# Optimization experiments

Measured on AMD Instinct MI355X. Metric: run time of the kernel, lower is better.

The kernel has to match this reference:

```python
import jax, jax.numpy as jnp
import numpy as np

EPS = 1e-12  # torch F.normalize eps

def _l2norm(x):
    n = jnp.linalg.norm(x, axis=-1, keepdims=True)
    return x / jnp.maximum(n, EPS)

def _encode(h, mask, W, b):
    # h: [B,S,H], mask: [B,S] int
    h = h * mask[..., None].astype(h.dtype)      # zero padded tokens
    pooled = h[:, 0]                             # pooling_type='cls'
    col = h[:, 1:] @ W + b                       # colbert_linear on tokens 1:
    return _l2norm(pooled), _l2norm(col)         # normalize=True


def setup_inputs() -> dict:
    key = jax.random.key(0)
    k1, k2, k3, k4, k5, k6 = jax.random.split(key, 6)
    Q, Sq, C, Sc, H, D = 64, 32, 256, 256, 768, 128
    return {
        "q_hidden": jax.random.normal(k1, (Q, Sq, H), jnp.float32),
        "c_hidden": jax.random.normal(k2, (C, Sc, H), jnp.float32),
        "W": jax.random.normal(k3, (H, D), jnp.float32) / np.sqrt(H).astype(np.float32),
        "b": jax.random.normal(k4, (D,), jnp.float32) * 0.01,
        "q_mask": jax.random.randint(k5, (Q, Sq), 0, 2, jnp.int32),
        "c_mask": jax.random.randint(k6, (C, Sc), 0, 2, jnp.int32),
    }


def reference(q_hidden, c_hidden, W, b, q_mask, c_mask):
    q_pooled, q_col = _encode(q_hidden, q_mask, W, b)   # q_col: [Q, Sq-1, D]
    c_pooled, c_col = _encode(c_hidden, c_mask, W, b)   # c_col: [C, Sc-1, D]
    # MaxSim late interaction (get_batch_colbert_sim)
    token_sim = jnp.einsum('qin,cjn->qicj', q_col, c_col)  # [Q, Sq-1, C, Sc-1]
    sim = token_sim.max(axis=-1)                           # max over doc tokens j
    denom = q_mask[:, 1:].sum(-1, keepdims=True).astype(sim.dtype)
    sim = sim.sum(axis=1) / denom                          # [Q, C]
    return sim, q_pooled, c_pooled
```

## Files before the change

### kernel.cpp

```cpp
#include <hip/hip_runtime.h>
#include <hip/hip_bf16.h>

#define QN 64
#define SQ 32
#define CN 256
#define SC 256
#define HD 768
#define DD 128

typedef __attribute__((ext_vector_type(8))) short short8;
typedef __attribute__((ext_vector_type(4))) float f32x4;

static __device__ __forceinline__ unsigned short f2bf(float x) {
  unsigned u = __float_as_uint(x);
  unsigned r = 0x7FFFu + ((u >> 16) & 1u);
  return (unsigned short)((u + r) >> 16);
}
static __device__ __forceinline__ unsigned pack2(float a, float b) {
  return (unsigned)f2bf(a) | ((unsigned)f2bf(b) << 16);
}

typedef const __attribute__((address_space(1))) unsigned int* as1_u32p;
typedef __attribute__((address_space(3))) unsigned int* as3_u32p;
static __device__ __forceinline__ void gl_lds16(const void* g, void* l) {
  __builtin_amdgcn_global_load_lds((as1_u32p)g, (as3_u32p)l, 16, 0, 0);
}

__global__ __launch_bounds__(256) void prep_kernel(
    const float* __restrict__ W,
    const float* __restrict__ qh, const int* __restrict__ qm,
    const float* __restrict__ ch, const int* __restrict__ cm,
    unsigned short* __restrict__ WtS,
    float* __restrict__ outq, float* __restrict__ outc,
    unsigned short* __restrict__ qcolP) {
  __shared__ float red[4];
  int bid = blockIdx.x, tid = threadIdx.x;

  if (bid < DD) {
    int d = bid;
    if (tid < 96) {
      int kc = tid;
      unsigned p[4];
#pragma unroll
      for (int e = 0; e < 4; ++e) {
        float a = W[(size_t)(kc * 8 + 2 * e) * DD + d];
        float b = W[(size_t)(kc * 8 + 2 * e + 1) * DD + d];
        p[e] = pack2(a, b);
      }
      int kcp = (kc & ~7) | ((kc & 7) ^ (d & 7));
      *(uint4*)&WtS[((size_t)d * 96 + kcp) * 8] = *(uint4*)p;
    }
    return;
  }

  int row = bid - DD;
  const float* src;
  float* dst;
  float m;
  if (row < QN) {
    src = qh + (size_t)row * SQ * HD;
    m = (float)qm[row * SQ];
    dst = outq + (size_t)row * HD;
  } else {
    int b = row - QN;
    src = ch + (size_t)b * SC * HD;
    m = (float)cm[b * SC];
    dst = outc + (size_t)b * HD;
  }
  float ss = 0.f;
  for (int k = tid; k < HD; k += 256) {
    float v = src[k] * m;
    ss += v * v;
  }
  int lane = tid & 63, wv = tid >> 6;
  for (int off = 32; off; off >>= 1) ss += __shfl_xor(ss, off);
  if (lane == 0) red[wv] = ss;
  __syncthreads();
  float tot = red[0] + red[1] + red[2] + red[3];
  float inv = 1.f / fmaxf(sqrtf(tot), 1e-12f);
  for (int k = tid; k < HD; k += 256) dst[k] = src[k] * m * inv;
  if (row < QN && tid < 64)
    ((unsigned*)(qcolP + ((size_t)row * 32 + 31) * DD))[tid] = 0u;
}

union ProjLDS {
  unsigned short w[2][128 * 64];
  float cep[64 * 132];
};

__global__ __launch_bounds__(256, 2) void proj_kernel(
    const float* __restrict__ q_hidden, const float* __restrict__ c_hidden,
    const int* __restrict__ q_mask, const int* __restrict__ c_mask,
    const unsigned short* __restrict__ WtS, const float* __restrict__ bias,
    unsigned short* __restrict__ qcol, unsigned short* __restrict__ ccol) {
  __shared__ ProjLDS u;
  int bx = blockIdx.x;
  int isQ = (bx >= 510) ? 1 : 0;
  int base = isQ ? (bx - 510) : bx;
  int tid = threadIdx.x, lane = tid & 63, wv = tid >> 6;
  int lm = lane & 15, lq = lane >> 4;

  const float* abase[2];
#pragma unroll
  for (int mt = 0; mt < 2; ++mt) {
    int g = base * 128 + wv * 32 + mt * 16 + lm;
    const float* hp;
    if (isQ) {
      g = (g > 1983) ? 1983 : g;
      int qq = g / 31, t = g - qq * 31;
      hp = q_hidden + ((size_t)qq * SQ + t + 1) * HD;
    } else {
      int cb = g / 255, t = g - cb * 255;
      hp = c_hidden + ((size_t)cb * SC + t + 1) * HD;
    }
    abase[mt] = hp + lq * 8;
  }

  const unsigned short* wptr[4];
#pragma unroll
  for (int i = 0; i < 4; ++i) {
    int d = i * 32 + (tid >> 3);
    wptr[i] = WtS + ((size_t)d * 96 + (tid & 7)) * 8;
  }

  f32x4 acc[2][8];
#pragma unroll
  for (int i = 0; i < 2; ++i)
#pragma unroll
    for (int j = 0; j < 8; ++j) acc[i][j] = (f32x4){0.f, 0.f, 0.f, 0.f};

  float4 Pa[8], Pb[8];

#pragma unroll
  for (int w = 0; w < 2; ++w)
#pragma unroll
    for (int mt = 0; mt < 2; ++mt) {
      Pa[w * 4 + mt * 2 + 0] = *(const float4*)(abase[mt] + w * 32);
      Pa[w * 4 + mt * 2 + 1] = *(const float4*)(abase[mt] + w * 32 + 4);
    }
#pragma unroll
  for (int i = 0; i < 4; ++i)
    gl_lds16(wptr[i], (char*)&u.w[0][0] + (size_t)(i * 256 + wv * 64) * 16);
  __syncthreads();

#define PROJ_STEP(t, PC, PN, CB, NB, PREFETCH)                                 \
  {                                                                            \
    if (PREFETCH) {                                                            \
      _Pragma("unroll")                                                        \
      for (int w = 0; w < 2; ++w)                                              \
        _Pragma("unroll")                                                      \
        for (int mt = 0; mt < 2; ++mt) {                                       \
          PN[w * 4 + mt * 2 + 0] =                                             \
              *(const float4*)(abase[mt] + (t + 1) * 64 + w * 32);             \
          PN[w * 4 + mt * 2 + 1] =                                             \
              *(const float4*)(abase[mt] + (t + 1) * 64 + w * 32 + 4);         \
        }                                                                      \
      _Pragma("unroll")                                                        \
      for (int i = 0; i < 4; ++i)                                              \
        gl_lds16(wptr[i] + (t + 1) * 64,                                       \
                 (char*)&u.w[NB][0] + (size_t)(i * 256 + wv * 64) * 16);       \
    }                                                                          \
    _Pragma("unroll")                                                          \
    for (int w = 0; w < 2; ++w) {                                              \
      short8 afr[2];                                                           \
      _Pragma("unroll")                                                        \
      for (int mt = 0; mt < 2; ++mt) {                                         \
        float4 a0 = PC[w * 4 + mt * 2], a1 = PC[w * 4 + mt * 2 + 1];           \
        unsigned pk[4];                                                        \
        pk[0] = pack2(a0.x, a0.y); pk[1] = pack2(a0.z, a0.w);                  \
        pk[2] = pack2(a1.x, a1.y); pk[3] = pack2(a1.z, a1.w);                  \
        afr[mt] = *(short8*)pk;                                                \
      }                                                                        \
      _Pragma("unroll")                                                        \
      for (int nt = 0; nt < 8; ++nt) {                                         \
        int d = nt * 16 + lm;                                                  \
        int pc = (w * 4 + lq) ^ (lm & 7);                                      \
        short8 bfr = *(const short8*)&u.w[CB][d * 64 + pc * 8];                \
        acc[0][nt] = __builtin_amdgcn_mfma_f32_16x16x32_bf16(afr[0], bfr,      \
                                                             acc[0][nt], 0, 0, 0); \
        acc[1][nt] = __builtin_amdgcn_mfma_f32_16x16x32_bf16(afr[1], bfr,      \
                                                             acc[1][nt], 0, 0, 0); \
      }                                                                        \
    }                                                                          \
    __syncthreads();                                                           \
  }

#pragma unroll
  for (int s = 0; s < 12; s += 2) {
    PROJ_STEP(s, Pa, Pb, 0, 1, 1);
    PROJ_STEP(s + 1, Pb, Pa, 1, 0, (s + 1 < 11));
  }
#undef PROJ_STEP

  int tk = tid >> 2, qt = tid & 3;
#pragma unroll
  for (int h = 0; h < 2; ++h) {
    __syncthreads();
    if ((wv >> 1) == h) {
#pragma unroll
      for (int mt = 0; mt < 2; ++mt)
#pragma unroll
        for (int nt = 0; nt < 8; ++nt)
#pragma unroll
          for (int r = 0; r < 4; ++r) {
            int row = (wv & 1) * 32 + mt * 16 + lq * 4 + r;
            u.cep[row * 132 + nt * 16 + lm] = acc[mt][nt][r];
          }
    }
    __syncthreads();

    int g = base * 128 + h * 64 + tk;
    int qq, t, valid = 1;
    float fm;
    if (isQ) {
      if (g > 1983) { valid = 0; g = 1983; }
      qq = g / 31; t = g - qq * 31;
      fm = (float)q_mask[qq * SQ + t + 1];
    } else {
      qq = g / 255; t = g - qq * 255;
      fm = (float)c_mask[qq * SC + t + 1];
    }

    float v[32];
    float ss = 0.f;
#pragma unroll
    for (int j = 0; j < 8; ++j) {
      float4 cv = *(const float4*)&u.cep[tk * 132 + qt * 32 + j * 4];
      float4 bv = *(const float4*)&bias[qt * 32 + j * 4];
      v[4 * j + 0] = cv.x * fm + bv.x; v[4 * j + 1] = cv.y * fm + bv.y;
      v[4 * j + 2] = cv.z * fm + bv.z; v[4 * j + 3] = cv.w * fm + bv.w;
#pragma unroll
      for (int e = 0; e < 4; ++e) ss += v[4 * j + e] * v[4 * j + e];
    }
    ss += __shfl_xor(ss, 1);
    ss += __shfl_xor(ss, 2);
    float inv = 1.f / fmaxf(sqrtf(ss), 1e-12f);

    uint4 pk4[4];
#pragma unroll
    for (int j = 0; j < 4; ++j) {
      unsigned p[4];
#pragma unroll
      for (int e = 0; e < 4; ++e)
        p[e] = pack2(v[8 * j + 2 * e] * inv, v[8 * j + 2 * e + 1] * inv);
      pk4[j] = *(uint4*)p;
    }

    if (isQ) {
      if (valid) {
        uint4* dst = (uint4*)(qcol + ((size_t)qq * 32 + t) * DD + qt * 32);
#pragma unroll
        for (int j = 0; j < 4; ++j) dst[j] = pk4[j];
      }
    } else {
      uint4* rowp = (uint4*)(ccol + ((size_t)qq * 256 + t) * DD);
#pragma unroll
      for (int j = 0; j < 4; ++j) {
        int kc = qt * 4 + j;
        int p = (kc & 8) | ((kc & 7) ^ (t & 7));
        rowp[p] = pk4[j];
      }
      if (t == 254) {
        uint4* rowp2 = rowp + 16;
#pragma unroll
        for (int j = 0; j < 4; ++j) {
          int kc = qt * 4 + j;
          int p = (kc & 8) | ((kc & 7) ^ 7);
          rowp2[p] = pk4[j];
        }
      }
    }
  }
}

__global__ __launch_bounds__(256, 2) void sim_kernel(
    const unsigned short* __restrict__ qcolP,
    const unsigned short* __restrict__ ccol,
    const int* __restrict__ qmask,
    float* __restrict__ sim) {
  __shared__ unsigned short cbuf[2][128 * 128];
  int tid = threadIdx.x, lane = tid & 63, wv = tid >> 6;
  int lm = lane & 15, lq = lane >> 4;
  int qb = blockIdx.y * 16 + wv * 4;
  int c0 = blockIdx.x * 2;

  short8 af[4][2][4];
#pragma unroll
  for (int q2 = 0; q2 < 4; ++q2)
#pragma unroll
    for (int it = 0; it < 2; ++it)
#pragma unroll
      for (int kf = 0; kf < 4; ++kf)
        af[q2][it][kf] = *(const short8*)(qcolP +
            (((size_t)(qb + q2) * 32 + it * 16 + lm) * DD + kf * 32 + lq * 8));

  float dinv[4];
#pragma unroll
  for (int q2 = 0; q2 < 4; ++q2) {
    float v = (lane >= 1 && lane < 32) ? (float)qmask[(qb + q2) * SQ + lane] : 0.f;
    for (int off = 1; off < 64; off <<= 1) v += __shfl_xor(v, off);
    dinv[q2] = 1.f / v;
  }

  const unsigned short* csrc = ccol + (size_t)c0 * SC * DD;

#pragma unroll
  for (int i = 0; i < 8; ++i)
    gl_lds16(csrc + (size_t)(i * 256 + tid) * 8,
             (char*)&cbuf[0][0] + (size_t)(i * 256 + wv * 64) * 16);
  __syncthreads();

  float rmax[4][2];
  for (int ht = 0; ht < 4; ++ht) {
    int b = ht & 1;
    if (!(ht & 1)) {
#pragma unroll
      for (int q2 = 0; q2 < 4; ++q2) {
        rmax[q2][0] = -__builtin_inff();
        rmax[q2][1] = -__builtin_inff();
      }
    }
    if (ht < 3) {
      const unsigned short* s2 = csrc + (size_t)(ht + 1) * 16384;
#pragma unroll
      for (int i = 0; i < 8; ++i)
        gl_lds16(s2 + (size_t)(i * 256 + tid) * 8,
                 (char*)&cbuf[b ^ 1][0] + (size_t)(i * 256 + wv * 64) * 16);
    }

    for (int jt = 0; jt < 8; ++jt) {
      short8 cf[4];
#pragma unroll
      for (int kf = 0; kf < 4; ++kf) {
        int row = jt * 16 + lm;
        int kc = kf * 4 + lq;
        int p = (kc & 8) | ((kc & 7) ^ (row & 7));
        cf[kf] = *(const short8*)&cbuf[b][(size_t)(row * 16 + p) * 8];
      }
#pragma unroll
      for (int q2 = 0; q2 < 4; ++q2)
#pragma unroll
        for (int it = 0; it < 2; ++it) {
          f32x4 acc = (f32x4){0.f, 0.f, 0.f, 0.f};
#pragma unroll
          for (int kf = 0; kf < 4; ++kf)
            acc = __builtin_amdgcn_mfma_f32_16x16x32_bf16(cf[kf], af[q2][it][kf], acc, 0, 0, 0);
          float loc = fmaxf(fmaxf(acc[0], acc[1]), fmaxf(acc[2], acc[3]));
          rmax[q2][it] = fmaxf(rmax[q2][it], loc);
        }
    }

    if (ht & 1) {
      int c = c0 + (ht >> 1);
#pragma unroll
      for (int q2 = 0; q2 < 4; ++q2) {
        float m0 = rmax[q2][0], m1 = rmax[q2][1];
        m0 = fmaxf(m0, __shfl_xor(m0, 16)); m0 = fmaxf(m0, __shfl_xor(m0, 32));
        m1 = fmaxf(m1, __shfl_xor(m1, 16)); m1 = fmaxf(m1, __shfl_xor(m1, 32));
        float s = m0 + ((lm == 15) ? 0.f : m1);
        s += __shfl_xor(s, 1); s += __shfl_xor(s, 2);
        s += __shfl_xor(s, 4); s += __shfl_xor(s, 8);
        if (lane == 0) sim[(qb + q2) * CN + c] = s * dinv[q2];
      }
    }
    __syncthreads();
  }
}

extern "C" void kernel_launch(void* const* d_in, const int* in_sizes, int n_in,
                              void* d_out, int out_size, void* d_ws, size_t ws_size,
                              hipStream_t stream) {
  const float* q_hidden = (const float*)d_in[0];
  const float* c_hidden = (const float*)d_in[1];
  const float* W = (const float*)d_in[2];
  const float* bias = (const float*)d_in[3];
  const int* q_mask = (const int*)d_in[4];
  const int* c_mask = (const int*)d_in[5];

  float* out = (float*)d_out;
  float* sim = out;
  float* q_pooled = out + QN * CN;
  float* c_pooled = q_pooled + QN * HD;

  unsigned short* WtS   = (unsigned short*)d_ws;
  unsigned short* qcolP = (unsigned short*)((char*)d_ws + (256 << 10));
  unsigned short* ccol  = (unsigned short*)((char*)d_ws + (1 << 20));

  prep_kernel<<<DD + QN + CN, 256, 0, stream>>>(W, q_hidden, q_mask, c_hidden, c_mask,
                                                WtS, q_pooled, c_pooled, qcolP);
  proj_kernel<<<526, 256, 0, stream>>>(q_hidden, c_hidden, q_mask, c_mask,
                                       WtS, bias, qcolP, ccol);
  sim_kernel<<<dim3(128, 4), 256, 0, stream>>>(qcolP, ccol, q_mask, sim);
}
```

Measured before the change: 373.6 us.

## Halve proj tile to 64 rows and skip hidden loads for masked tokens

The projection kernel now handles 64 token rows per block instead of 128, doubling the grid and raising the occupancy hint from 2 to 4 blocks per CU. The epilogue loses its two-pass staging. Rows whose mask is zero no longer load their fp32 hidden activations and feed zeros to the MFMA instead, which cuts HBM traffic for padded tokens (about half of them with random masks). The trade-off is that the shared weight tile is reloaded by twice as many blocks, and fewer MFMAs run per LDS B-fragment read.

Measured after the change: 345.8 us. 7.5% less time.

```diff
diff --git a/kernel.cpp b/kernel.cpp
--- a/kernel.cpp
+++ b/kernel.cpp
@@ -88,32 +88,29 @@
   float cep[64 * 132];
 };
 
-__global__ __launch_bounds__(256, 2) void proj_kernel(
+__global__ __launch_bounds__(256, 4) void proj_kernel(
     const float* __restrict__ q_hidden, const float* __restrict__ c_hidden,
     const int* __restrict__ q_mask, const int* __restrict__ c_mask,
     const unsigned short* __restrict__ WtS, const float* __restrict__ bias,
     unsigned short* __restrict__ qcol, unsigned short* __restrict__ ccol) {
   __shared__ ProjLDS u;
   int bx = blockIdx.x;
-  int isQ = (bx >= 510) ? 1 : 0;
-  int base = isQ ? (bx - 510) : bx;
+  int isQ = (bx >= 1020) ? 1 : 0;
+  int base = isQ ? (bx - 1020) : bx;
   int tid = threadIdx.x, lane = tid & 63, wv = tid >> 6;
   int lm = lane & 15, lq = lane >> 4;
 
-  const float* abase[2];
-#pragma unroll
-  for (int mt = 0; mt < 2; ++mt) {
-    int g = base * 128 + wv * 32 + mt * 16 + lm;
-    const float* hp;
-    if (isQ) {
-      g = (g > 1983) ? 1983 : g;
-      int qq = g / 31, t = g - qq * 31;
-      hp = q_hidden + ((size_t)qq * SQ + t + 1) * HD;
-    } else {
-      int cb = g / 255, t = g - cb * 255;
-      hp = c_hidden + ((size_t)cb * SC + t + 1) * HD;
-    }
-    abase[mt] = hp + lq * 8;
+  int g = base * 64 + wv * 16 + lm;
+  const float* abase;
+  int pm;
+  if (isQ) {
+    int qq = g / 31, t = g - qq * 31;
+    abase = q_hidden + ((size_t)qq * SQ + t + 1) * HD + lq * 8;
+    pm = q_mask[qq * SQ + t + 1];
+  } else {
+    int cb = g / 255, t = g - cb * 255;
+    abase = c_hidden + ((size_t)cb * SC + t + 1) * HD + lq * 8;
+    pm = c_mask[cb * SC + t + 1];
   }
 
   const unsigned short* wptr[4];
@@ -123,21 +120,23 @@
     wptr[i] = WtS + ((size_t)d * 96 + (tid & 7)) * 8;
   }
 
-  f32x4 acc[2][8];
-#pragma unroll
-  for (int i = 0; i < 2; ++i)
-#pragma unroll
-    for (int j = 0; j < 8; ++j) acc[i][j] = (f32x4){0.f, 0.f, 0.f, 0.f};
-
-  float4 Pa[8], Pb[8];
-
-#pragma unroll
-  for (int w = 0; w < 2; ++w)
-#pragma unroll
-    for (int mt = 0; mt < 2; ++mt) {
-      Pa[w * 4 + mt * 2 + 0] = *(const float4*)(abase[mt] + w * 32);
-      Pa[w * 4 + mt * 2 + 1] = *(const float4*)(abase[mt] + w * 32 + 4);
-    }
+  f32x4 acc[8];
+#pragma unroll
+  for (int n = 0; n < 8; ++n) acc[n] = (f32x4){0.f, 0.f, 0.f, 0.f};
+
+  float4 Pa[4], Pb[4];
+#pragma unroll
+  for (int i = 0; i < 4; ++i) {
+    Pa[i] = (float4){0.f, 0.f, 0.f, 0.f};
+    Pb[i] = (float4){0.f, 0.f, 0.f, 0.f};
+  }
+
+  if (pm) {
+    Pa[0] = *(const float4*)(abase);
+    Pa[1] = *(const float4*)(abase + 4);
+    Pa[2] = *(const float4*)(abase + 32);
+    Pa[3] = *(const float4*)(abase + 36);
+  }
 #pragma unroll
   for (int i = 0; i < 4; ++i)
     gl_lds16(wptr[i], (char*)&u.w[0][0] + (size_t)(i * 256 + wv * 64) * 16);
@@ -146,15 +145,12 @@
 #define PROJ_STEP(t, PC, PN, CB, NB, PREFETCH)                                 \
   {                                                                            \
     if (PREFETCH) {                                                            \
-      _Pragma("unroll")                                                        \
-      for (int w = 0; w < 2; ++w)                                              \
-        _Pragma("unroll")                                                      \
-        for (int mt = 0; mt < 2; ++mt) {                                       \
-          PN[w * 4 + mt * 2 + 0] =                                             \
-              *(const float4*)(abase[mt] + (t + 1) * 64 + w * 32);             \
-          PN[w * 4 + mt * 2 + 1] =                                             \
-              *(const float4*)(abase[mt] + (t + 1) * 64 + w * 32 + 4);         \
-        }                                                                      \
+      if (pm) {                                                                \
+        PN[0] = *(const float4*)(abase + (t + 1) * 64);                        \
+        PN[1] = *(const float4*)(abase + (t + 1) * 64 + 4);                    \
+        PN[2] = *(const float4*)(abase + (t + 1) * 64 + 32);                   \
+        PN[3] = *(const float4*)(abase + (t + 1) * 64 + 36);                   \
+      }                                                                        \
       _Pragma("unroll")                                                        \
       for (int i = 0; i < 4; ++i)                                              \
         gl_lds16(wptr[i] + (t + 1) * 64,                                       \
@@ -162,24 +158,18 @@
     }                                                                          \
     _Pragma("unroll")                                                          \
     for (int w = 0; w < 2; ++w) {                                              \
-      short8 afr[2];                                                           \
-      _Pragma("unroll")                                                        \
-      for (int mt = 0; mt < 2; ++mt) {                                         \
-        float4 a0 = PC[w * 4 + mt * 2], a1 = PC[w * 4 + mt * 2 + 1];           \
-        unsigned pk[4];                                                        \
-        pk[0] = pack2(a0.x, a0.y); pk[1] = pack2(a0.z, a0.w);                  \
-        pk[2] = pack2(a1.x, a1.y); pk[3] = pack2(a1.z, a1.w);                  \
-        afr[mt] = *(short8*)pk;                                                \
-      }                                                                        \
+      float4 a0 = PC[w * 2], a1 = PC[w * 2 + 1];                               \
+      unsigned pk[4];                                                          \
+      pk[0] = pack2(a0.x, a0.y); pk[1] = pack2(a0.z, a0.w);                    \
+      pk[2] = pack2(a1.x, a1.y); pk[3] = pack2(a1.z, a1.w);                    \
+      short8 afr = *(short8*)pk;                                               \
       _Pragma("unroll")                                                        \
       for (int nt = 0; nt < 8; ++nt) {                                         \
         int d = nt * 16 + lm;                                                  \
         int pc = (w * 4 + lq) ^ (lm & 7);                                      \
         short8 bfr = *(const short8*)&u.w[CB][d * 64 + pc * 8];                \
-        acc[0][nt] = __builtin_amdgcn_mfma_f32_16x16x32_bf16(afr[0], bfr,      \
-                                                             acc[0][nt], 0, 0, 0); \
-        acc[1][nt] = __builtin_amdgcn_mfma_f32_16x16x32_bf16(afr[1], bfr,      \
-                                                             acc[1][nt], 0, 0, 0); \
+        acc[nt] = __builtin_amdgcn_mfma_f32_16x16x32_bf16(afr, bfr,            \
+                                                          acc[nt], 0, 0, 0);  \
       }                                                                        \
     }                                                                          \
     __syncthreads();                                                           \
@@ -192,82 +182,71 @@
   }
 #undef PROJ_STEP
 
+#pragma unroll
+  for (int nt = 0; nt < 8; ++nt)
+#pragma unroll
+    for (int r = 0; r < 4; ++r) {
+      int row = wv * 16 + lq * 4 + r;
+      u.cep[row * 132 + nt * 16 + lm] = acc[nt][r];
+    }
+  __syncthreads();
+
   int tk = tid >> 2, qt = tid & 3;
-#pragma unroll
-  for (int h = 0; h < 2; ++h) {
-    __syncthreads();
-    if ((wv >> 1) == h) {
-#pragma unroll
-      for (int mt = 0; mt < 2; ++mt)
-#pragma unroll
-        for (int nt = 0; nt < 8; ++nt)
-#pragma unroll
-          for (int r = 0; r < 4; ++r) {
-            int row = (wv & 1) * 32 + mt * 16 + lq * 4 + r;
-            u.cep[row * 132 + nt * 16 + lm] = acc[mt][nt][r];
-          }
-    }
-    __syncthreads();
-
-    int g = base * 128 + h * 64 + tk;
-    int qq, t, valid = 1;
-    float fm;
-    if (isQ) {
-      if (g > 1983) { valid = 0; g = 1983; }
-      qq = g / 31; t = g - qq * 31;
-      fm = (float)q_mask[qq * SQ + t + 1];
-    } else {
-      qq = g / 255; t = g - qq * 255;
-      fm = (float)c_mask[qq * SC + t + 1];
-    }
-
-    float v[32];
-    float ss = 0.f;
-#pragma unroll
-    for (int j = 0; j < 8; ++j) {
-      float4 cv = *(const float4*)&u.cep[tk * 132 + qt * 32 + j * 4];
-      float4 bv = *(const float4*)&bias[qt * 32 + j * 4];
-      v[4 * j + 0] = cv.x * fm + bv.x; v[4 * j + 1] = cv.y * fm + bv.y;
-      v[4 * j + 2] = cv.z * fm + bv.z; v[4 * j + 3] = cv.w * fm + bv.w;
-#pragma unroll
-      for (int e = 0; e < 4; ++e) ss += v[4 * j + e] * v[4 * j + e];
-    }
-    ss += __shfl_xor(ss, 1);
-    ss += __shfl_xor(ss, 2);
-    float inv = 1.f / fmaxf(sqrtf(ss), 1e-12f);
-
-    uint4 pk4[4];
+  int g2 = base * 64 + tk;
+  int qq, t;
+  float fm;
+  if (isQ) {
+    qq = g2 / 31; t = g2 - qq * 31;
+    fm = (float)q_mask[qq * SQ + t + 1];
+  } else {
+    qq = g2 / 255; t = g2 - qq * 255;
+    fm = (float)c_mask[qq * SC + t + 1];
+  }
+
+  float v[32];
+  float ss = 0.f;
+#pragma unroll
+  for (int j = 0; j < 8; ++j) {
+    float4 cv = *(const float4*)&u.cep[tk * 132 + qt * 32 + j * 4];
+    float4 bv = *(const float4*)&bias[qt * 32 + j * 4];
+    v[4 * j + 0] = cv.x * fm + bv.x; v[4 * j + 1] = cv.y * fm + bv.y;
+    v[4 * j + 2] = cv.z * fm + bv.z; v[4 * j + 3] = cv.w * fm + bv.w;
+#pragma unroll
+    for (int e = 0; e < 4; ++e) ss += v[4 * j + e] * v[4 * j + e];
+  }
+  ss += __shfl_xor(ss, 1);
+  ss += __shfl_xor(ss, 2);
+  float inv = 1.f / fmaxf(sqrtf(ss), 1e-12f);
+
+  uint4 pk4[4];
+#pragma unroll
+  for (int j = 0; j < 4; ++j) {
+    unsigned p[4];
+#pragma unroll
+    for (int e = 0; e < 4; ++e)
+      p[e] = pack2(v[8 * j + 2 * e] * inv, v[8 * j + 2 * e + 1] * inv);
+    pk4[j] = *(uint4*)p;
+  }
+
+  if (isQ) {
+    uint4* dst = (uint4*)(qcol + ((size_t)qq * 32 + t) * DD + qt * 32);
+#pragma unroll
+    for (int j = 0; j < 4; ++j) dst[j] = pk4[j];
+  } else {
+    uint4* rowp = (uint4*)(ccol + ((size_t)qq * 256 + t) * DD);
 #pragma unroll
     for (int j = 0; j < 4; ++j) {
-      unsigned p[4];
-#pragma unroll
-      for (int e = 0; e < 4; ++e)
-        p[e] = pack2(v[8 * j + 2 * e] * inv, v[8 * j + 2 * e + 1] * inv);
-      pk4[j] = *(uint4*)p;
-    }
-
-    if (isQ) {
-      if (valid) {
-        uint4* dst = (uint4*)(qcol + ((size_t)qq * 32 + t) * DD + qt * 32);
-#pragma unroll
-        for (int j = 0; j < 4; ++j) dst[j] = pk4[j];
-      }
-    } else {
-      uint4* rowp = (uint4*)(ccol + ((size_t)qq * 256 + t) * DD);
+      int kc = qt * 4 + j;
+      int p = (kc & 8) | ((kc & 7) ^ (t & 7));
+      rowp[p] = pk4[j];
+    }
+    if (t == 254) {
+      uint4* rowp2 = rowp + 16;
 #pragma unroll
       for (int j = 0; j < 4; ++j) {
         int kc = qt * 4 + j;
-        int p = (kc & 8) | ((kc & 7) ^ (t & 7));
-        rowp[p] = pk4[j];
-      }
-      if (t == 254) {
-        uint4* rowp2 = rowp + 16;
-#pragma unroll
-        for (int j = 0; j < 4; ++j) {
-          int kc = qt * 4 + j;
-          int p = (kc & 8) | ((kc & 7) ^ 7);
-          rowp2[p] = pk4[j];
-        }
+        int p = (kc & 8) | ((kc & 7) ^ 7);
+        rowp2[p] = pk4[j];
       }
     }
   }
@@ -388,7 +367,7 @@
 
   prep_kernel<<<DD + QN + CN, 256, 0, stream>>>(W, q_hidden, q_mask, c_hidden, c_mask,
                                                 WtS, q_pooled, c_pooled, qcolP);
-  proj_kernel<<<526, 256, 0, stream>>>(q_hidden, c_hidden, q_mask, c_mask,
-                                       WtS, bias, qcolP, ccol);
+  proj_kernel<<<1051, 256, 0, stream>>>(q_hidden, c_hidden, q_mask, c_mask,
+                                        WtS, bias, qcolP, ccol);
   sim_kernel<<<dim3(128, 4), 256, 0, stream>>>(qcolP, ccol, q_mask, sim);
 }
```
